# Performance work log

Hardware: AMD Instinct MI355X
Metric: run time of the kernel (lower is better)

## Reference

```python
import jax, jax.numpy as jnp
import numpy as np


def setup_inputs() -> dict:
    key = jax.random.key(0)
    k1, k2, k3, k4 = jax.random.split(key, 4)
    S, D, DKQ, DV = 8192, 2048, 128, 128
    x = jax.random.normal(k1, (S, D), dtype=jnp.float32)
    w_q = jax.random.uniform(k2, (D, DKQ), dtype=jnp.float32)
    w_k = jax.random.uniform(k3, (D, DKQ), dtype=jnp.float32)
    w_v = jax.random.uniform(k4, (D, DV), dtype=jnp.float32)
    return {"x": x, "w_q": w_q, "w_k": w_k, "w_v": w_v}


def reference(x, w_q, w_k, w_v):
    # x: [S, D]; single-head causal attention, unbatched as in the source.
    dim_kq = w_q.shape[1]
    q = x @ w_q  # [S, DKQ]
    k = x @ w_k  # [S, DKQ]
    v = x @ w_v  # [S, DV]
    scores = (q @ k.T) / jnp.sqrt(jnp.asarray(dim_kq, q.dtype))  # [S, S]
    S = scores.shape[0]
    causal = jnp.tril(jnp.ones((S, S), dtype=bool))
    scores = jnp.where(causal, scores, -jnp.inf)
    att_w = jax.nn.softmax(scores, axis=-1)
    return att_w @ v  # [S, DV]
```

## Files before the change

### kernel.cpp

```cpp
#include <hip/hip_runtime.h>

#define S_LEN 8192
#define D_DIM 2048
#define HD    128
#define KVB   32
#define NCH   16
#define QTR   256

typedef __attribute__((ext_vector_type(8))) short bf16x8;
typedef __attribute__((ext_vector_type(4))) float f32x4;

__device__ __forceinline__ unsigned short f2bf(float f) {
  unsigned int u = __float_as_uint(f);
  u += 0x7fffu + ((u >> 16) & 1u);
  return (unsigned short)(u >> 16);
}
__device__ __forceinline__ float bf2f(unsigned short h) {
  return __uint_as_float(((unsigned int)h) << 16);
}

__device__ __forceinline__ void glds16(const void* g, const short* l) {
  __builtin_amdgcn_global_load_lds(
      (const __attribute__((address_space(1))) void*)g,
      (__attribute__((address_space(3))) void*)l, 16, 0, 0);
}

__global__ __launch_bounds__(256)
void split_x_kernel(const float* __restrict__ x,
                    unsigned short* __restrict__ xh, unsigned short* __restrict__ xl)
{
  const size_t n4 = (size_t)S_LEN * D_DIM / 4;
  size_t idx = (size_t)blockIdx.x * 256 + threadIdx.x;
  const size_t stride = (size_t)gridDim.x * 256;
  for (; idx < n4; idx += stride) {
    float4 v = ((const float4*)x)[idx];
    ushort4 h, l;
#pragma unroll
    for (int j = 0; j < 4; ++j) {
      float f = ((const float*)&v)[j];
      unsigned short hb = f2bf(f);
      ((unsigned short*)&h)[j] = hb;
      ((unsigned short*)&l)[j] = f2bf(f - bf2f(hb));
    }
    ((ushort4*)xh)[idx] = h;
    ((ushort4*)xl)[idx] = l;
  }
}

__global__ __launch_bounds__(256)
void split_w_kernel(const float* __restrict__ wq, const float* __restrict__ wk,
                    const float* __restrict__ wv,
                    unsigned short* __restrict__ wTh, unsigned short* __restrict__ wTl)
{
  const int mode = blockIdx.y;
  const float* __restrict__ w = (mode == 0) ? wq : (mode == 1) ? wk : wv;
  unsigned short* __restrict__ oh = wTh + (size_t)mode * HD * D_DIM;
  unsigned short* __restrict__ ol = wTl + (size_t)mode * HD * D_DIM;
  const int k0 = blockIdx.x * 64;

  __shared__ float ws[64][132];
  const int t = threadIdx.x;
#pragma unroll
  for (int i = 0; i < 8; ++i) {
    int idx = t + i * 256;
    int row = idx >> 5;
    int c4  = idx & 31;
    *(float4*)&ws[row][c4 * 4] = *(const float4*)(w + (size_t)(k0 + row) * HD + c4 * 4);
  }
  __syncthreads();
#pragma unroll
  for (int i = 0; i < 4; ++i) {
    int task = t + i * 256;
    int col = task >> 3;
    int kc  = task & 7;
    ushort4 h[2], l[2];
#pragma unroll
    for (int e = 0; e < 8; ++e) {
      float f = ws[kc * 8 + e][col];
      unsigned short hb = f2bf(f);
      ((unsigned short*)&h[e >> 2])[e & 3] = hb;
      ((unsigned short*)&l[e >> 2])[e & 3] = f2bf(f - bf2f(hb));
    }
    size_t off = (size_t)col * D_DIM + k0 + kc * 8;
    *(ushort4*)(oh + off)     = h[0];
    *(ushort4*)(oh + off + 4) = h[1];
    *(ushort4*)(ol + off)     = l[0];
    *(ushort4*)(ol + off + 4) = l[1];
  }
}

__global__ __launch_bounds__(256)
void proj_kernel(const unsigned short* __restrict__ xh, const unsigned short* __restrict__ xl,
                 const unsigned short* __restrict__ wTh, const unsigned short* __restrict__ wTl,
                 unsigned short* __restrict__ q_hi, unsigned short* __restrict__ q_lo,
                 unsigned short* __restrict__ k_hi, unsigned short* __restrict__ k_lo,
                 unsigned short* __restrict__ vT)
{
  __shared__ short sm[2][12288];

  const int mode = blockIdx.y;
  const int mt   = blockIdx.x;
  const bool split = (mode < 2);

  const unsigned short* gxh = xh + (size_t)mt * 64 * D_DIM;
  const unsigned short* gxl = xl + (size_t)mt * 64 * D_DIM;
  const unsigned short* gwh = wTh + (size_t)mode * HD * D_DIM;
  const unsigned short* gwl = wTl + (size_t)mode * HD * D_DIM;

  const int t   = threadIdx.x;
  const int wid = t >> 6;
  const int ln  = t & 63;
  const int cl  = ln & 15;
  const int g4  = ln >> 4;

  auto stage = [&](int kt, int buf) {
    short* b = sm[buf];
    {
      int slot = wid * 64 + ln;
      int row = slot >> 2, sc = slot & 3;
      int kof = (sc ^ (row & 3)) * 8;
      glds16(gxh + (size_t)row * D_DIM + kt + kof, b + wid * 512);
      if (split)
        glds16(gxl + (size_t)row * D_DIM + kt + kof, b + 2048 + wid * 512);
    }
#pragma unroll
    for (int g = 0; g < 2; ++g) {
      int slot = g * 256 + wid * 64 + ln;
      int col = slot >> 2, sc = slot & 3;
      int kof = (sc ^ (col & 3)) * 8;
      glds16(gwh + (size_t)col * D_DIM + kt + kof, b + 4096 + (g * 256 + wid * 64) * 8);
      if (split)
        glds16(gwl + (size_t)col * D_DIM + kt + kof, b + 8192 + (g * 256 + wid * 64) * 8);
    }
  };

  f32x4 acc[2][4];
#pragma unroll
  for (int m = 0; m < 2; ++m)
#pragma unroll
    for (int n = 0; n < 4; ++n) acc[m][n] = f32x4{0.f, 0.f, 0.f, 0.f};

  stage(0, 0);
  __syncthreads();

  for (int kt = 0, step = 0; kt < D_DIM; kt += 32, ++step) {
    const int cur = step & 1;
    if (kt + 32 < D_DIM) stage(kt + 32, cur ^ 1);

    const short* b = sm[cur];
    bf16x8 a_h[2], a_l[2], b_h[4], b_l[4];
#pragma unroll
    for (int m = 0; m < 2; ++m) {
      int row = (wid >> 1) * 32 + m * 16 + cl;
      int byte = row * 64 + ((g4 ^ (row & 3)) << 4);
      a_h[m] = *(const bf16x8*)((const char*)b + byte);
      if (split) a_l[m] = *(const bf16x8*)((const char*)b + 4096 + byte);
    }
#pragma unroll
    for (int n = 0; n < 4; ++n) {
      int col = (wid & 1) * 64 + n * 16 + cl;
      int byte = col * 64 + ((g4 ^ (col & 3)) << 4);
      b_h[n] = *(const bf16x8*)((const char*)b + 8192 + byte);
      if (split) b_l[n] = *(const bf16x8*)((const char*)b + 16384 + byte);
    }

#pragma unroll
    for (int m = 0; m < 2; ++m)
#pragma unroll
      for (int n = 0; n < 4; ++n)
        acc[m][n] = __builtin_amdgcn_mfma_f32_16x16x32_bf16(a_h[m], b_h[n], acc[m][n], 0, 0, 0);
    if (split) {
#pragma unroll
      for (int m = 0; m < 2; ++m)
#pragma unroll
        for (int n = 0; n < 4; ++n) {
          acc[m][n] = __builtin_amdgcn_mfma_f32_16x16x32_bf16(a_l[m], b_h[n], acc[m][n], 0, 0, 0);
          acc[m][n] = __builtin_amdgcn_mfma_f32_16x16x32_bf16(a_h[m], b_l[n], acc[m][n], 0, 0, 0);
        }
    }
    __syncthreads();
  }

  const int rbase = mt * 64 + (wid >> 1) * 32 + g4 * 4;
  const int cbase = (wid & 1) * 64 + cl;

  if (mode < 2) {
    const float scale = (mode == 0) ? 0.08838834764831843f : 1.0f;
    unsigned short* __restrict__ oh = (mode == 0) ? q_hi : k_hi;
    unsigned short* __restrict__ ol = (mode == 0) ? q_lo : k_lo;
#pragma unroll
    for (int m = 0; m < 2; ++m)
#pragma unroll
      for (int n = 0; n < 4; ++n)
#pragma unroll
        for (int r = 0; r < 4; ++r) {
          float val = acc[m][n][r] * scale;
          unsigned short hb = f2bf(val);
          size_t off = (size_t)(rbase + m * 16 + r) * HD + cbase + n * 16;
          oh[off] = hb;
          ol[off] = f2bf(val - bf2f(hb));
        }
  } else {
#pragma unroll
    for (int m = 0; m < 2; ++m)
#pragma unroll
      for (int n = 0; n < 4; ++n) {
        ushort4 o;
#pragma unroll
        for (int r = 0; r < 4; ++r) ((unsigned short*)&o)[r] = f2bf(acc[m][n][r]);
        int col = cbase + n * 16;
        *(ushort4*)(vT + (size_t)col * S_LEN + rbase + m * 16) = o;
      }
  }
}

__global__ __launch_bounds__(512)
void attn_kernel(const unsigned short* __restrict__ q_hi, const unsigned short* __restrict__ q_lo,
                 const unsigned short* __restrict__ k_hi, const unsigned short* __restrict__ k_lo,
                 const unsigned short* __restrict__ vT,
                 unsigned short* __restrict__ part_o, float* __restrict__ part_ml)
{
  extern __shared__ short smem[];
  short* ls_kh = smem;
  short* ls_kl = ls_kh + 8192;
  short* ls_v  = ls_kl + 8192;
  short* ls_ql = ls_v + 8192;
  short* ls_p  = ls_ql + 32768;

  const int t   = threadIdx.x;
  const int wid = t >> 6;
  const int ln  = t & 63;
  const int cl  = ln & 15;
  const int g4  = ln >> 4;
  const int pairId = blockIdx.x >> 4;
  const int chunk  = blockIdx.x & 15;

  short* pw = ls_p + wid * 1280;

  auto stage = [&](int j, int buf) {
    const unsigned short* gkh = k_hi + (size_t)j * KVB * HD;
    const unsigned short* gkl = k_lo + (size_t)j * KVB * HD;
    const unsigned short* gv  = vT + (size_t)j * KVB;
    {
      int row = t >> 4, sc = t & 15;
      int c16 = sc ^ (row & 7);
      glds16(gkh + row * HD + c16 * 8, ls_kh + buf * 4096 + t * 8);
      glds16(gkl + row * HD + c16 * 8, ls_kl + buf * 4096 + t * 8);
    }
    {
      int d = t >> 2, sub = t & 3;
      int s2 = sub ^ ((d >> 1) & 3);
      glds16(gv + (size_t)d * S_LEN + s2 * 8, ls_v + buf * 4096 + t * 8);
    }
  };

  for (int hh = 0; hh < 2; ++hh) {
    const int T = hh ? (31 - pairId) : pairId;
    const int jmaxB = 8 * T + 7;
    const int jmaxW = 8 * T + wid;
    const int rowbase = T * QTR + wid * 32;

    {
      const unsigned short* gql = q_lo + (size_t)T * QTR * HD;
#pragma unroll
      for (int i = 0; i < 8; ++i) {
        int slot = i * 512 + t;
        int row = slot >> 4, sc = slot & 15;
        int c16 = sc ^ (row & 7);
        glds16(gql + (size_t)row * HD + c16 * 8, ls_ql + slot * 8);
      }
    }

    bf16x8 qh[2][4];
#pragma unroll
    for (int rg = 0; rg < 2; ++rg) {
      const size_t qoff = ((size_t)rowbase + rg * 16 + cl) * HD + g4 * 8;
#pragma unroll
      for (int kc = 0; kc < 4; ++kc)
        qh[rg][kc] = *(const bf16x8*)(q_hi + qoff + kc * 32);
    }

    float m_i[2][4], l_i[2][4];
    f32x4 o_acc[2][8];
#pragma unroll
    for (int rg = 0; rg < 2; ++rg)
#pragma unroll
      for (int i = 0; i < 4; ++i) { m_i[rg][i] = -1e30f; l_i[rg][i] = 0.f; }
#pragma unroll
    for (int rg = 0; rg < 2; ++rg)
#pragma unroll
      for (int c2 = 0; c2 < 8; ++c2) o_acc[rg][c2] = f32x4{0.f, 0.f, 0.f, 0.f};

    if (chunk <= jmaxB) {
      int cur = 0;
      stage(chunk, 0);
      __syncthreads();
      for (int j = chunk; j <= jmaxB; j += NCH) {
        if (j + NCH <= jmaxB) stage(j + NCH, cur ^ 1);

        if (j <= jmaxW) {
          const int rl0 = wid * 32 + cl;
          const int rl1 = rl0 + 16;
          f32x4 s[2][2];
          s[0][0] = f32x4{0.f, 0.f, 0.f, 0.f};
          s[0][1] = f32x4{0.f, 0.f, 0.f, 0.f};
          s[1][0] = f32x4{0.f, 0.f, 0.f, 0.f};
          s[1][1] = f32x4{0.f, 0.f, 0.f, 0.f};
          __builtin_amdgcn_s_setprio(1);
#pragma unroll
          for (int kc = 0; kc < 4; ++kc) {
            const int ch = kc * 4 + g4;
            bf16x8 ql0 = *(const bf16x8*)((const char*)ls_ql + rl0 * 256 + ((ch ^ (rl0 & 7)) << 4));
            bf16x8 ql1 = *(const bf16x8*)((const char*)ls_ql + rl1 * 256 + ((ch ^ (rl1 & 7)) << 4));
#pragma unroll
            for (int c = 0; c < 2; ++c) {
              const int kcol = c * 16 + cl;
              const int byteK = kcol * 256 + ((ch ^ (kcol & 7)) << 4);
              bf16x8 khf = *(const bf16x8*)((const char*)(ls_kh + cur * 4096) + byteK);
              bf16x8 klf = *(const bf16x8*)((const char*)(ls_kl + cur * 4096) + byteK);
              s[0][c] = __builtin_amdgcn_mfma_f32_16x16x32_bf16(qh[0][kc], khf, s[0][c], 0, 0, 0);
              s[0][c] = __builtin_amdgcn_mfma_f32_16x16x32_bf16(ql0,      khf, s[0][c], 0, 0, 0);
              s[0][c] = __builtin_amdgcn_mfma_f32_16x16x32_bf16(qh[0][kc], klf, s[0][c], 0, 0, 0);
              s[1][c] = __builtin_amdgcn_mfma_f32_16x16x32_bf16(qh[1][kc], khf, s[1][c], 0, 0, 0);
              s[1][c] = __builtin_amdgcn_mfma_f32_16x16x32_bf16(ql1,      khf, s[1][c], 0, 0, 0);
              s[1][c] = __builtin_amdgcn_mfma_f32_16x16x32_bf16(qh[1][kc], klf, s[1][c], 0, 0, 0);
            }
          }
          __builtin_amdgcn_s_setprio(0);

          if (j == jmaxW) {
#pragma unroll
            for (int rg = 0; rg < 2; ++rg)
#pragma unroll
              for (int c = 0; c < 2; ++c)
#pragma unroll
                for (int i = 0; i < 4; ++i) {
                  int col = j * KVB + c * 16 + cl;
                  int row = rowbase + rg * 16 + g4 * 4 + i;
                  if (col > row) s[rg][c][i] = -1e30f;
                }
          }

          bool ok = true;
#pragma unroll
          for (int rg = 0; rg < 2; ++rg)
#pragma unroll
            for (int i = 0; i < 4; ++i) {
              float mx = fmaxf(s[rg][0][i], s[rg][1][i]);
              ok = ok && (mx <= m_i[rg][i] + 8.0f);
            }
          if (!__all(ok)) {
#pragma unroll
            for (int rg = 0; rg < 2; ++rg)
#pragma unroll
              for (int i = 0; i < 4; ++i) {
                float rm = fmaxf(s[rg][0][i], s[rg][1][i]);
                rm = fmaxf(rm, __shfl_xor(rm, 1));
                rm = fmaxf(rm, __shfl_xor(rm, 2));
                rm = fmaxf(rm, __shfl_xor(rm, 4));
                rm = fmaxf(rm, __shfl_xor(rm, 8));
                float mnew = fmaxf(m_i[rg][i], rm);
                float corr = __expf(m_i[rg][i] - mnew);
                l_i[rg][i] *= corr;
#pragma unroll
                for (int c2 = 0; c2 < 8; ++c2) o_acc[rg][c2][i] *= corr;
                m_i[rg][i] = mnew;
              }
          }

#pragma unroll
          for (int rg = 0; rg < 2; ++rg)
#pragma unroll
            for (int c = 0; c < 2; ++c)
#pragma unroll
              for (int i = 0; i < 4; ++i) {
                float sv = s[rg][c][i];
                float p = (sv > -1e29f) ? __expf(sv - m_i[rg][i]) : 0.f;
                l_i[rg][i] += p;
                pw[(rg * 16 + g4 * 4 + i) * 40 + c * 16 + cl] = (short)f2bf(p);
              }

          bf16x8 pa0 = *(const bf16x8*)((const char*)pw + cl * 80 + g4 * 16);
          bf16x8 pa1 = *(const bf16x8*)((const char*)pw + (16 + cl) * 80 + g4 * 16);
          __builtin_amdgcn_s_setprio(1);
#pragma unroll
          for (int c2 = 0; c2 < 8; ++c2) {
            const int d0 = c2 * 16 + cl;
            const int byteV = d0 * 64 + ((g4 ^ ((d0 >> 1) & 3)) << 4);
            bf16x8 vb = *(const bf16x8*)((const char*)(ls_v + cur * 4096) + byteV);
            o_acc[0][c2] = __builtin_amdgcn_mfma_f32_16x16x32_bf16(pa0, vb, o_acc[0][c2], 0, 0, 0);
            o_acc[1][c2] = __builtin_amdgcn_mfma_f32_16x16x32_bf16(pa1, vb, o_acc[1][c2], 0, 0, 0);
          }
          __builtin_amdgcn_s_setprio(0);
        }

        __syncthreads();
        cur ^= 1;
      }
    }

    const int base = T * NCH + chunk;
#pragma unroll
    for (int rg = 0; rg < 2; ++rg)
#pragma unroll
      for (int c2 = 0; c2 < 8; ++c2)
#pragma unroll
        for (int i = 0; i < 4; ++i) {
          int row = wid * 32 + rg * 16 + g4 * 4 + i;
          part_o[((size_t)base * QTR + row) * HD + c2 * 16 + cl] = f2bf(o_acc[rg][c2][i]);
        }

#pragma unroll
    for (int rg = 0; rg < 2; ++rg)
#pragma unroll
      for (int i = 0; i < 4; ++i) {
        float lv = l_i[rg][i];
        lv += __shfl_xor(lv, 1);
        lv += __shfl_xor(lv, 2);
        lv += __shfl_xor(lv, 4);
        lv += __shfl_xor(lv, 8);
        if (cl == 0) {
          int row = wid * 32 + rg * 16 + g4 * 4 + i;
          part_ml[base * 512 + row]       = m_i[rg][i];
          part_ml[base * 512 + 256 + row] = lv;
        }
      }
  }
}

__global__ __launch_bounds__(128)
void merge_kernel(const unsigned short* __restrict__ part_o, const float* __restrict__ part_ml,
                  float* __restrict__ out)
{
  const int row = blockIdx.x;
  const int T   = row >> 8;
  const int r   = row & 255;
  const int c   = threadIdx.x;

  float m[NCH], l[NCH];
  float mstar = -3e38f;
#pragma unroll
  for (int s = 0; s < NCH; ++s) {
    m[s] = part_ml[(T * NCH + s) * 512 + r];
    l[s] = part_ml[(T * NCH + s) * 512 + 256 + r];
    mstar = fmaxf(mstar, m[s]);
  }
  float num = 0.f, den = 0.f;
#pragma unroll
  for (int s = 0; s < NCH; ++s) {
    float wgt = __expf(m[s] - mstar);
    den += l[s] * wgt;
    num += wgt * bf2f(part_o[((size_t)(T * NCH + s) * QTR + r) * HD + c]);
  }
  out[(size_t)row * HD + c] = num / den;
}

extern "C" void kernel_launch(void* const* d_in, const int* in_sizes, int n_in,
                              void* d_out, int out_size, void* d_ws, size_t ws_size,
                              hipStream_t stream)
{
  const float* x  = (const float*)d_in[0];
  const float* wq = (const float*)d_in[1];
  const float* wk = (const float*)d_in[2];
  const float* wv = (const float*)d_in[3];
  float* out = (float*)d_out;

  unsigned short* p = (unsigned short*)d_ws;
  unsigned short* xh = p;  p += (size_t)S_LEN * D_DIM;
  unsigned short* xl = p;  p += (size_t)S_LEN * D_DIM;
  unsigned short* wTh = p; p += (size_t)3 * HD * D_DIM;
  unsigned short* wTl = p; p += (size_t)3 * HD * D_DIM;
  unsigned short* q_hi = p; p += (size_t)S_LEN * HD;
  unsigned short* q_lo = p; p += (size_t)S_LEN * HD;
  unsigned short* k_hi = p; p += (size_t)S_LEN * HD;
  unsigned short* k_lo = p; p += (size_t)S_LEN * HD;
  unsigned short* vT   = p; p += (size_t)S_LEN * HD;
  unsigned short* part_o = xh;
  float* part_ml = (float*)wTh;

  split_x_kernel<<<4096, 256, 0, stream>>>(x, xh, xl);
  split_w_kernel<<<dim3(32, 3), 256, 0, stream>>>(wq, wk, wv, wTh, wTl);
  proj_kernel<<<dim3(128, 3), 256, 0, stream>>>(xh, xl, wTh, wTl,
                                                q_hi, q_lo, k_hi, k_lo, vT);
  const int smem_bytes = (8192 * 3 + 32768 + 8 * 1280) * (int)sizeof(short);
  attn_kernel<<<dim3(256), 512, smem_bytes, stream>>>(q_hi, q_lo, k_hi, k_lo, vT,
                                                      part_o, part_ml);
  merge_kernel<<<dim3(8192), 128, 0, stream>>>(part_o, part_ml, out);
}
```

Baseline: 147.0 us.

## Fuse x bf16 split into projection load and triple-buffer attention K/V staging

Removes the standalone split_x kernel. The projection kernel now reads fp32 x directly into registers and converts it to hi/lo bf16 inside its k-loop, writing the result to LDS after the MFMAs. This avoids writing and re-reading the large xh/xl intermediates through HBM. Separately, the attention kernel moves from double to triple buffering of K/V tiles, using explicit vmcnt waits and raw barriers so global loads run two steps ahead. The cost is more LDS per block and conversion ALU work inside the projection loop.

```diff
diff --git a/kernel.cpp b/kernel.cpp
--- a/kernel.cpp
+++ b/kernel.cpp
@@ -23,28 +23,6 @@
   __builtin_amdgcn_global_load_lds(
       (const __attribute__((address_space(1))) void*)g,
       (__attribute__((address_space(3))) void*)l, 16, 0, 0);
-}
-
-__global__ __launch_bounds__(256)
-void split_x_kernel(const float* __restrict__ x,
-                    unsigned short* __restrict__ xh, unsigned short* __restrict__ xl)
-{
-  const size_t n4 = (size_t)S_LEN * D_DIM / 4;
-  size_t idx = (size_t)blockIdx.x * 256 + threadIdx.x;
-  const size_t stride = (size_t)gridDim.x * 256;
-  for (; idx < n4; idx += stride) {
-    float4 v = ((const float4*)x)[idx];
-    ushort4 h, l;
-#pragma unroll
-    for (int j = 0; j < 4; ++j) {
-      float f = ((const float*)&v)[j];
-      unsigned short hb = f2bf(f);
-      ((unsigned short*)&h)[j] = hb;
-      ((unsigned short*)&l)[j] = f2bf(f - bf2f(hb));
-    }
-    ((ushort4*)xh)[idx] = h;
-    ((ushort4*)xl)[idx] = l;
-  }
 }
 
 __global__ __launch_bounds__(256)
@@ -90,7 +68,7 @@
 }
 
 __global__ __launch_bounds__(256)
-void proj_kernel(const unsigned short* __restrict__ xh, const unsigned short* __restrict__ xl,
+void proj_kernel(const float* __restrict__ x,
                  const unsigned short* __restrict__ wTh, const unsigned short* __restrict__ wTl,
                  unsigned short* __restrict__ q_hi, unsigned short* __restrict__ q_lo,
                  unsigned short* __restrict__ k_hi, unsigned short* __restrict__ k_lo,
@@ -102,8 +80,6 @@
   const int mt   = blockIdx.x;
   const bool split = (mode < 2);
 
-  const unsigned short* gxh = xh + (size_t)mt * 64 * D_DIM;
-  const unsigned short* gxl = xl + (size_t)mt * 64 * D_DIM;
   const unsigned short* gwh = wTh + (size_t)mode * HD * D_DIM;
   const unsigned short* gwl = wTl + (size_t)mode * HD * D_DIM;
 
@@ -113,16 +89,13 @@
   const int cl  = ln & 15;
   const int g4  = ln >> 4;
 
-  auto stage = [&](int kt, int buf) {
+  const int slotx = wid * 64 + ln;
+  const int rowx  = slotx >> 2, scx = slotx & 3;
+  const int kofx  = (scx ^ (rowx & 3)) * 8;
+  const float* gx = x + (size_t)(mt * 64 + rowx) * D_DIM + kofx;
+
+  auto stagew = [&](int kt, int buf) {
     short* b = sm[buf];
-    {
-      int slot = wid * 64 + ln;
-      int row = slot >> 2, sc = slot & 3;
-      int kof = (sc ^ (row & 3)) * 8;
-      glds16(gxh + (size_t)row * D_DIM + kt + kof, b + wid * 512);
-      if (split)
-        glds16(gxl + (size_t)row * D_DIM + kt + kof, b + 2048 + wid * 512);
-    }
 #pragma unroll
     for (int g = 0; g < 2; ++g) {
       int slot = g * 256 + wid * 64 + ln;
@@ -133,6 +106,21 @@
         glds16(gwl + (size_t)col * D_DIM + kt + kof, b + 8192 + (g * 256 + wid * 64) * 8);
     }
   };
+  auto writex = [&](const float4& a0, const float4& a1, int buf) {
+    short* b = sm[buf];
+    float fv[8];
+    *(float4*)&fv[0] = a0;
+    *(float4*)&fv[4] = a1;
+    bf16x8 hv, lv;
+#pragma unroll
+    for (int e = 0; e < 8; ++e) {
+      unsigned short hb = f2bf(fv[e]);
+      hv[e] = (short)hb;
+      lv[e] = (short)f2bf(fv[e] - bf2f(hb));
+    }
+    *(bf16x8*)(b + slotx * 8) = hv;
+    if (split) *(bf16x8*)(b + 2048 + slotx * 8) = lv;
+  };
 
   f32x4 acc[2][4];
 #pragma unroll
@@ -140,12 +128,23 @@
 #pragma unroll
     for (int n = 0; n < 4; ++n) acc[m][n] = f32x4{0.f, 0.f, 0.f, 0.f};
 
-  stage(0, 0);
+  {
+    float4 a0 = *(const float4*)(gx + 0);
+    float4 a1 = *(const float4*)(gx + 4);
+    stagew(0, 0);
+    writex(a0, a1, 0);
+  }
   __syncthreads();
 
   for (int kt = 0, step = 0; kt < D_DIM; kt += 32, ++step) {
     const int cur = step & 1;
-    if (kt + 32 < D_DIM) stage(kt + 32, cur ^ 1);
+    const bool more = (kt + 32 < D_DIM);
+    float4 n0, n1;
+    if (more) {
+      n0 = *(const float4*)(gx + kt + 32);
+      n1 = *(const float4*)(gx + kt + 36);
+      stagew(kt + 32, cur ^ 1);
+    }
 
     const short* b = sm[cur];
     bf16x8 a_h[2], a_l[2], b_h[4], b_l[4];
@@ -178,6 +177,7 @@
           acc[m][n] = __builtin_amdgcn_mfma_f32_16x16x32_bf16(a_h[m], b_l[n], acc[m][n], 0, 0, 0);
         }
     }
+    if (more) writex(n0, n1, cur ^ 1);
     __syncthreads();
   }
 
@@ -222,10 +222,10 @@
 {
   extern __shared__ short smem[];
   short* ls_kh = smem;
-  short* ls_kl = ls_kh + 8192;
-  short* ls_v  = ls_kl + 8192;
-  short* ls_ql = ls_v + 8192;
-  short* ls_p  = ls_ql + 32768;
+  short* ls_kl = smem + 12288;
+  short* ls_v  = smem + 24576;
+  short* ls_ql = smem + 36864;
+  short* ls_p  = smem + 69632;
 
   const int t   = threadIdx.x;
   const int wid = t >> 6;
@@ -292,15 +292,25 @@
       for (int c2 = 0; c2 < 8; ++c2) o_acc[rg][c2] = f32x4{0.f, 0.f, 0.f, 0.f};
 
     if (chunk <= jmaxB) {
-      int cur = 0;
+      const int nsteps = (jmaxB - chunk) / NCH + 1;
       stage(chunk, 0);
-      __syncthreads();
-      for (int j = chunk; j <= jmaxB; j += NCH) {
-        if (j + NCH <= jmaxB) stage(j + NCH, cur ^ 1);
+      { int j1 = (nsteps > 1) ? chunk + NCH : chunk; stage(j1, 1); }
+      asm volatile("s_waitcnt vmcnt(3)" ::: "memory");
+      __builtin_amdgcn_s_barrier();
+
+      int bcur = 0, bstg = 2;
+      for (int k = 0; k < nsteps; ++k) {
+        const int j = chunk + k * NCH;
+        int jn = chunk + (k + 2) * NCH;
+        if (jn > jmaxB) jn = jmaxB;
+        stage(jn, bstg);
 
         if (j <= jmaxW) {
           const int rl0 = wid * 32 + cl;
           const int rl1 = rl0 + 16;
+          const short* bkh = ls_kh + bcur * 4096;
+          const short* bkl = ls_kl + bcur * 4096;
+          const short* bv  = ls_v  + bcur * 4096;
           f32x4 s[2][2];
           s[0][0] = f32x4{0.f, 0.f, 0.f, 0.f};
           s[0][1] = f32x4{0.f, 0.f, 0.f, 0.f};
@@ -316,8 +326,8 @@
             for (int c = 0; c < 2; ++c) {
               const int kcol = c * 16 + cl;
               const int byteK = kcol * 256 + ((ch ^ (kcol & 7)) << 4);
-              bf16x8 khf = *(const bf16x8*)((const char*)(ls_kh + cur * 4096) + byteK);
-              bf16x8 klf = *(const bf16x8*)((const char*)(ls_kl + cur * 4096) + byteK);
+              bf16x8 khf = *(const bf16x8*)((const char*)bkh + byteK);
+              bf16x8 klf = *(const bf16x8*)((const char*)bkl + byteK);
               s[0][c] = __builtin_amdgcn_mfma_f32_16x16x32_bf16(qh[0][kc], khf, s[0][c], 0, 0, 0);
               s[0][c] = __builtin_amdgcn_mfma_f32_16x16x32_bf16(ql0,      khf, s[0][c], 0, 0, 0);
               s[0][c] = __builtin_amdgcn_mfma_f32_16x16x32_bf16(qh[0][kc], klf, s[0][c], 0, 0, 0);
@@ -387,15 +397,17 @@
           for (int c2 = 0; c2 < 8; ++c2) {
             const int d0 = c2 * 16 + cl;
             const int byteV = d0 * 64 + ((g4 ^ ((d0 >> 1) & 3)) << 4);
-            bf16x8 vb = *(const bf16x8*)((const char*)(ls_v + cur * 4096) + byteV);
+            bf16x8 vb = *(const bf16x8*)((const char*)bv + byteV);
             o_acc[0][c2] = __builtin_amdgcn_mfma_f32_16x16x32_bf16(pa0, vb, o_acc[0][c2], 0, 0, 0);
             o_acc[1][c2] = __builtin_amdgcn_mfma_f32_16x16x32_bf16(pa1, vb, o_acc[1][c2], 0, 0, 0);
           }
           __builtin_amdgcn_s_setprio(0);
         }
 
-        __syncthreads();
-        cur ^= 1;
+        asm volatile("s_waitcnt vmcnt(3) lgkmcnt(0)" ::: "memory");
+        __builtin_amdgcn_s_barrier();
+        bcur = (bcur == 2) ? 0 : bcur + 1;
+        bstg = (bstg == 2) ? 0 : bstg + 1;
       }
     }
 
@@ -478,11 +490,10 @@
   unsigned short* part_o = xh;
   float* part_ml = (float*)wTh;
 
-  split_x_kernel<<<4096, 256, 0, stream>>>(x, xh, xl);
   split_w_kernel<<<dim3(32, 3), 256, 0, stream>>>(wq, wk, wv, wTh, wTl);
-  proj_kernel<<<dim3(128, 3), 256, 0, stream>>>(xh, xl, wTh, wTl,
+  proj_kernel<<<dim3(128, 3), 256, 0, stream>>>(x, wTh, wTl,
                                                 q_hi, q_lo, k_hi, k_lo, vT);
-  const int smem_bytes = (8192 * 3 + 32768 + 8 * 1280) * (int)sizeof(short);
+  const int smem_bytes = (12288 * 3 + 32768 + 8 * 1280) * (int)sizeof(short);
   attn_kernel<<<dim3(256), 512, smem_bytes, stream>>>(q_hi, q_lo, k_hi, k_lo, vT,
                                                       part_o, part_ml);
   merge_kernel<<<dim3(8192), 128, 0, stream>>>(part_o, part_ml, out);
```

Result: faster. 138.6 us (-5.7%).
